# Kernel tuning notes

Measured on AMD Instinct MI355X. Metric: run time of the kernel, lower is better.

The kernel has to match this reference:

```python
import jax, jax.numpy as jnp
import numpy as np

B, N, F, H = 4, 1024, 1024, 16
D = F // H  # head_dim = 64


def setup_inputs() -> dict:
    key = jax.random.key(0)
    ks = jax.random.split(key, 12)
    s = 1.0 / np.sqrt(F)
    return {
        "feature_map": jax.random.normal(ks[0], (B, N, F), jnp.float32),
        "scene_token": jax.random.normal(ks[1], (B, F), jnp.float32),
        "relation_matrix": jax.random.normal(ks[2], (2 * N, 2 * N), jnp.float32) * 0.05,
        "Wq": jax.random.normal(ks[3], (F, F), jnp.float32) * s,
        "bq": jnp.zeros((F,), jnp.float32),
        "Wk": jax.random.normal(ks[4], (F, F), jnp.float32) * s,
        "bk": jnp.zeros((F,), jnp.float32),
        "Wv": jax.random.normal(ks[5], (F, F), jnp.float32) * s,
        "bv": jnp.zeros((F,), jnp.float32),
        "Wo": jax.random.normal(ks[6], (F, F), jnp.float32) * s,
        "bo": jnp.zeros((F,), jnp.float32),
    }


def reference(feature_map, scene_token, relation_matrix, Wq, bq, Wk, bk, Wv, bv, Wo, bo):
    b, n, f = feature_map.shape
    # scene token broadcast to n copies, concatenated -> [b, 2n, f]
    scene = jnp.broadcast_to(scene_token[:, None, :], (b, n, f))
    x = jnp.concatenate([scene, feature_map], axis=1)  # [b, 2n, f]
    q = (x @ Wq.T + bq).reshape(b, -1, H, D)
    k = (x @ Wk.T + bk).reshape(b, -1, H, D)
    v = (x @ Wv.T + bv).reshape(b, -1, H, D)
    scores = jnp.einsum("bqhd,bkhd->bhqk", q, k) / jnp.sqrt(jnp.float32(D))
    scores = scores + relation_matrix[None, None, :, :]
    weights = jax.nn.softmax(scores, axis=-1)
    attn = jnp.einsum("bhqk,bkhd->bqhd", weights, v).reshape(b, -1, f)
    return attn @ Wo.T + bo
```

## Files before the change

kernel.cpp:

```cpp
#include <hip/hip_runtime.h>
#include <hip/hip_bf16.h>
#include <cstdint>

typedef __hip_bfloat16 bf16;
typedef __attribute__((ext_vector_type(8))) short short8;
typedef __attribute__((ext_vector_type(4))) float f32x4;
typedef __attribute__((ext_vector_type(2))) unsigned int uint2v;

#define MFMA16(a, b, c) __builtin_amdgcn_mfma_f32_16x16x32_bf16((a), (b), (c), 0, 0, 0)

__device__ __forceinline__ void gl2lds16(const void* g, void* l) {
  __builtin_amdgcn_global_load_lds(
      (const __attribute__((address_space(1))) unsigned int*)g,
      (__attribute__((address_space(3))) unsigned int*)l,
      16, 0, 0);
}

__device__ __forceinline__ unsigned int pkcvt(float a, float b) {
  unsigned int r;
  asm("v_cvt_pk_bf16_f32 %0, %1, %2" : "=v"(r) : "v"(a), "v"(b));
  return r;
}

__device__ __forceinline__ uint2v plswap32(unsigned a, unsigned b) {
#if __has_builtin(__builtin_amdgcn_permlane32_swap)
  return __builtin_amdgcn_permlane32_swap(a, b, false, false);
#else
  const unsigned ax = __shfl_xor((int)a, 32), bx = __shfl_xor((int)b, 32);
  const bool hi = (threadIdx.x & 32) != 0;
  uint2v r;
  r[0] = hi ? bx : a;
  r[1] = hi ? b : ax;
  return r;
#endif
}

__device__ __forceinline__ uint2v plswap16(unsigned a, unsigned b) {
#if __has_builtin(__builtin_amdgcn_permlane16_swap)
  return __builtin_amdgcn_permlane16_swap(a, b, false, false);
#else
  const unsigned ax = __shfl_xor((int)a, 16), bx = __shfl_xor((int)b, 16);
  const bool hi = (threadIdx.x & 16) != 0;
  uint2v r;
  r[0] = hi ? bx : a;
  r[1] = hi ? b : ax;
  return r;
#endif
}

template <int V> struct IC { static constexpr int value = V; };

template <int WRITE_BF16>
__global__ __launch_bounds__(256) void gemm_bt(
    const bf16* __restrict__ A, const bf16* __restrict__ Bt,
    const float* __restrict__ bias, bf16* __restrict__ outb,
    float* __restrict__ outf, int M, int N, int K) {
  __shared__ bf16 sA[128 * 64];
  __shared__ bf16 sB[128 * 64];
  const int tid = threadIdx.x, w = tid >> 6, lane = tid & 63;
  const int n16 = lane & 15, quad = lane >> 4;
  const int mBase = blockIdx.y * 128, nBase = blockIdx.x * 128;
  const int wr = w >> 1, wc = w & 1;

  f32x4 acc[4][4];
#pragma unroll
  for (int mi = 0; mi < 4; mi++)
#pragma unroll
    for (int ni = 0; ni < 4; ni++) acc[mi][ni] = (f32x4){0.f, 0.f, 0.f, 0.f};

  const bf16* ag[4];
  const bf16* bg[4];
#pragma unroll
  for (int i = 0; i < 4; i++) {
    const int e = (i * 256 + tid) * 8;
    const int row = e >> 6, c0 = e & 63;
    const int col = c0 ^ ((row & 7) << 3);
    ag[i] = A + (size_t)(mBase + row) * K + col;
    bg[i] = Bt + (size_t)(nBase + row) * K + col;
  }
  const int u = (quad * 16) ^ ((n16 & 7) << 4);
  const int a0 = (wr * 64 + n16) * 128 + u;
  const int b0 = (wc * 64 + n16) * 128 + u;
  const char* const sAB = (const char*)sA;
  const char* const sBB = (const char*)sB;

  for (int k0 = 0; k0 < K; k0 += 64) {
    __syncthreads();
#pragma unroll
    for (int i = 0; i < 4; i++) {
      gl2lds16(ag[i] + k0, sA + i * 2048 + w * 512);
      gl2lds16(bg[i] + k0, sB + i * 2048 + w * 512);
    }
    __syncthreads();

#pragma unroll
    for (int kk = 0; kk < 2; kk++) {
      short8 af[4], bfg[4];
#pragma unroll
      for (int t = 0; t < 4; t++) {
        af[t] = *(const short8*)(sAB + (a0 ^ (kk << 6)) + t * 2048);
        bfg[t] = *(const short8*)(sBB + (b0 ^ (kk << 6)) + t * 2048);
      }
#pragma unroll
      for (int mi = 0; mi < 4; mi++)
#pragma unroll
        for (int ni = 0; ni < 4; ni++)
          acc[mi][ni] = MFMA16(af[mi], bfg[ni], acc[mi][ni]);
    }
  }

#pragma unroll
  for (int mi = 0; mi < 4; mi++)
#pragma unroll
    for (int ni = 0; ni < 4; ni++)
#pragma unroll
      for (int r = 0; r < 4; r++) {
        const int row = mBase + wr * 64 + mi * 16 + quad * 4 + r;
        const int col = nBase + wc * 64 + ni * 16 + n16;
        const float v = acc[mi][ni][r] + bias[col];
        if (WRITE_BF16)
          outb[(size_t)row * N + col] = __float2bfloat16(v);
        else
          outf[(size_t)row * N + col] = v;
      }
}

__global__ __launch_bounds__(256) void flash_kernel(
    const bf16* __restrict__ qkv, const float* __restrict__ relf,
    bf16* __restrict__ attn) {
  constexpr int S = 2048, R3 = 3072;
  __shared__ __align__(16) char smem[32768];
  bf16* const sK = (bf16*)smem;
  char* const sVtB = smem + 16384;

  const int tid = threadIdx.x, w = tid >> 6, lane = tid & 63;
  const int n16 = lane & 15, quad = lane >> 4;
  const int qt = blockIdx.x & 15;
  const int bh = blockIdx.x >> 4;
  const int h = bh & 15, b = bh >> 4;
  const int qb = qt * 128 + w * 32;
  const size_t rowbase = (size_t)b * S;
  const float SC = 0.125f * 1.44269504f;
  const size_t TADV = (size_t)64 * R3;

  short8 qf[2][2];
#pragma unroll
  for (int mi = 0; mi < 2; mi++) {
    const bf16* qp = qkv + (rowbase + qb + mi * 16 + n16) * R3 + h * 64;
#pragma unroll
    for (int c = 0; c < 2; c++) qf[mi][c] = *(const short8*)(qp + c * 32 + quad * 8);
  }

  f32x4 ot[4][2];
#pragma unroll
  for (int nc = 0; nc < 4; nc++)
#pragma unroll
    for (int mi = 0; mi < 2; mi++) ot[nc][mi] = (f32x4){0.f, 0.f, 0.f, 0.f};
  float l_lane[2] = {0.f, 0.f};

  const bf16* kg0;
  const bf16* kg1;
  {
    const int e0 = tid * 8;
    const int e1 = (256 + tid) * 8;
    const int k0r = e0 >> 6, c00 = e0 & 63;
    const int k1r = e1 >> 6, c01 = e1 & 63;
    kg0 = qkv + (rowbase + k0r) * R3 + 1024 + h * 64 + (c00 ^ ((k0r & 7) << 3));
    kg1 = qkv + (rowbase + k1r) * R3 + 1024 + h * 64 + (c01 ^ ((k1r & 7) << 3));
  }
  const int kldsoff = w * 512;

  const int kb0 = n16 * 128 + ((quad * 16) ^ ((n16 & 7) << 4));
  const int kb1 = kb0 ^ 64;
  const char* const sKB = (const char*)sK;

  const int kp = lane & 31;
  const int vd0 = w * 16 + (lane >> 5) * 8;
  const int kp4 = kp * 4;
  const bf16* vp = qkv + (rowbase + 2 * kp) * R3 + 2048 + h * 64 + vd0;

  const int vb0 = 128 * n16 + ((16 * quad) ^ ((n16 & 7) << 4));
  const int vb1 = vb0 ^ 64;

  short8 v0, v1;
  auto vstage = [&](int bufbyte) {
    const unsigned* a1 = (const unsigned*)&v1;
    const unsigned* a0 = (const unsigned*)&v0;
#pragma unroll
    for (int j = 0; j < 4; j++) {
      const unsigned lo = __builtin_amdgcn_perm(a1[j], a0[j], 0x05040100u);
      const unsigned hi = __builtin_amdgcn_perm(a1[j], a0[j], 0x07060302u);
      *(unsigned*)(sVtB + bufbyte + 128 * (vd0 + 2 * j) + (kp4 ^ ((2 * j) << 4))) = lo;
      *(unsigned*)(sVtB + bufbyte + 128 * (vd0 + 2 * j + 1) + (kp4 ^ ((2 * j + 1) << 4))) = hi;
    }
  };

  gl2lds16(kg0, sK + kldsoff);
  gl2lds16(kg1, sK + kldsoff + 2048);
  kg0 += TADV;
  kg1 += TADV;

  v0 = *(const short8*)vp;
  v1 = *(const short8*)(vp + R3);
  vstage(0);
  vp += TADV;
  v0 = *(const short8*)vp;
  v1 = *(const short8*)(vp + R3);
  vp += TADV;

  float4 rv[8];
  const float4* rpA = (const float4*)relf + (size_t)(qt * 32) * 2048 + w * 512 + lane;
  const float4* rpB = rpA + 256;
#pragma unroll
  for (int j = 0; j < 4; j++) {
    rv[j] = rpA[j * 64];
    rv[4 + j] = rpB[j * 64];
  }
  rpA += 2048;
  rpB += 2048;

  auto step = [&](auto curc, bool dodma, bool dovpf) {
    constexpr int CUR = decltype(curc)::value;
    constexpr int NXT = CUR ^ 1;
    __syncthreads();

    if (dodma) {
      gl2lds16(kg0, sK + NXT * 4096 + kldsoff);
      kg0 += TADV;
      gl2lds16(kg1, sK + NXT * 4096 + kldsoff + 2048);
      kg1 += TADV;
      vstage(NXT * 8192);
    }

#pragma unroll
    for (int kc = 0; kc < 2; kc++) {
      f32x4 st[2][2];
#pragma unroll
      for (int t2 = 0; t2 < 2; t2++) {
        const int kt4 = 2 * kc + t2;
        short8 kf[2];
        kf[0] = *(const short8*)(sKB + CUR * 8192 + kt4 * 2048 + kb0);
        kf[1] = *(const short8*)(sKB + CUR * 8192 + kt4 * 2048 + kb1);
#pragma unroll
        for (int mi = 0; mi < 2; mi++) {
          f32x4 z = (f32x4){0.f, 0.f, 0.f, 0.f};
          z = MFMA16(kf[0], qf[mi][0], z);
          z = MFMA16(kf[1], qf[mi][1], z);
          st[t2][mi] = z;
        }
      }
      if (kc == 0 && dovpf) {
        v0 = *(const short8*)vp;
        v1 = *(const short8*)(vp + R3);
        vp += TADV;
      }
      short8 pb[2];
#pragma unroll
      for (int mi = 0; mi < 2; mi++) {
        float acc = 0.f;
        unsigned d[2][2];
#pragma unroll
        for (int t2 = 0; t2 < 2; t2++) {
          const float4 rr = rv[mi * 4 + 2 * kc + t2];
          float p0 = __builtin_amdgcn_exp2f(fmaf(st[t2][mi][0], SC, rr.x));
          float p1 = __builtin_amdgcn_exp2f(fmaf(st[t2][mi][1], SC, rr.y));
          float p2 = __builtin_amdgcn_exp2f(fmaf(st[t2][mi][2], SC, rr.z));
          float p3 = __builtin_amdgcn_exp2f(fmaf(st[t2][mi][3], SC, rr.w));
          acc += (p0 + p1) + (p2 + p3);
          d[t2][0] = pkcvt(p0, p1);
          d[t2][1] = pkcvt(p2, p3);
        }
        l_lane[mi] += acc;
        const uint2v e0 = plswap32(d[0][0], d[1][0]);
        const uint2v e1 = plswap32(d[0][1], d[1][1]);
        const uint2v f0 = plswap16(e0[0], e0[1]);
        const uint2v f1 = plswap16(e1[0], e1[1]);
        union { short8 s; unsigned u[4]; } P;
        P.u[0] = f0[0]; P.u[1] = f1[0]; P.u[2] = f0[1]; P.u[3] = f1[1];
        pb[mi] = P.s;
      }
      if (kc == 1 && dodma) {
#pragma unroll
        for (int j = 0; j < 4; j++) {
          rv[j] = rpA[j * 64];
          rv[4 + j] = rpB[j * 64];
        }
        rpA += 2048;
        rpB += 2048;
      }
      short8 va[4];
#pragma unroll
      for (int nc = 0; nc < 4; nc++)
        va[nc] = *(const short8*)(sVtB + CUR * 8192 + 2048 * nc +
                                  (kc ? vb1 : vb0));
#pragma unroll
      for (int nc = 0; nc < 4; nc++)
#pragma unroll
        for (int mi = 0; mi < 2; mi++)
          ot[nc][mi] = MFMA16(va[nc], pb[mi], ot[nc][mi]);
    }
  };

#pragma unroll 1
  for (int t = 0; t < 16; t++) {
    const bool g = (t < 15);
    step(IC<0>{}, true, g);
    step(IC<1>{}, g, g);
  }

  float inv[2];
#pragma unroll
  for (int mi = 0; mi < 2; mi++) {
    float l = l_lane[mi];
    l += __shfl_xor(l, 16);
    l += __shfl_xor(l, 32);
    inv[mi] = 1.0f / l;
  }
  __syncthreads();
  bf16* const sEp = (bf16*)smem + w * (32 * 72);
#pragma unroll
  for (int mi = 0; mi < 2; mi++)
#pragma unroll
    for (int nc = 0; nc < 4; nc++) {
      uint2 pk;
      pk.x = pkcvt(ot[nc][mi][0] * inv[mi], ot[nc][mi][1] * inv[mi]);
      pk.y = pkcvt(ot[nc][mi][2] * inv[mi], ot[nc][mi][3] * inv[mi]);
      *(uint2*)(&sEp[(mi * 16 + n16) * 72 + nc * 16 + quad * 4]) = pk;
    }
#pragma unroll
  for (int t = 0; t < 4; t++) {
    const int row = t * 8 + (lane >> 3);
    const int dcol = (lane & 7) * 8;
    const short8 vrow = *(const short8*)(&sEp[row * 72 + dcol]);
    *(short8*)(attn + (rowbase + qb + row) * 1024 + h * 64 + dcol) = vrow;
  }
}

__global__ void prep_main(const float* __restrict__ fm, const float* __restrict__ scene,
                          const float* __restrict__ Wq, const float* __restrict__ Wk,
                          const float* __restrict__ Wv, const float* __restrict__ Wo,
                          const float* __restrict__ bq, const float* __restrict__ bk,
                          const float* __restrict__ bv, bf16* __restrict__ wW,
                          bf16* __restrict__ wWo, float* __restrict__ bC,
                          bf16* __restrict__ x) {
  const int blk = blockIdx.x;
  if (blk < 4096) {
    const int sel = blk >> 10;
    const int i = (((blk & 1023) * 256) + threadIdx.x) * 4;
    const float* src = (sel == 0) ? Wq : (sel == 1) ? Wk : (sel == 2) ? Wv : Wo;
    bf16* dst = (sel < 3) ? (wW + ((size_t)sel << 20) + i) : (wWo + i);
    const float4 v = *(const float4*)(src + i);
    dst[0] = __float2bfloat16(v.x);
    dst[1] = __float2bfloat16(v.y);
    dst[2] = __float2bfloat16(v.z);
    dst[3] = __float2bfloat16(v.w);
    if (blk == 0) {
      for (int z = threadIdx.x; z < 3072; z += 256)
        bC[z] = (z < 1024) ? bq[z] : (z < 2048) ? bk[z - 1024] : bv[z - 2048];
    }
  } else {
    const int bx = blk - 4096;
    const size_t i = ((size_t)bx * 256 + threadIdx.x) * 4;
    const int r = (int)(i >> 10), c = (int)(i & 1023);
    const int b = r >> 11, s = r & 2047;
    const float* src = (s < 1024)
                           ? (scene + ((size_t)b << 10) + c)
                           : (fm + (((size_t)b * 1024 + (s - 1024)) << 10) + c);
    const float4 v = *(const float4*)src;
    bf16* d = x + i;
    d[0] = __float2bfloat16(v.x);
    d[1] = __float2bfloat16(v.y);
    d[2] = __float2bfloat16(v.z);
    d[3] = __float2bfloat16(v.w);
  }
}

__global__ void prep_rel(const float* __restrict__ rel, float* __restrict__ relf) {
  const int idx = blockIdx.x * 256 + threadIdx.x;
  const int lane = idx & 63;
  const int j = (idx >> 6) & 7;
  const int w = (idx >> 9) & 3;
  const int kt = (idx >> 11) & 31;
  const int qt = idx >> 16;
  const int n16 = lane & 15, quad = lane >> 4;
  const int mi = j >> 2, kt4 = j & 3;
  const int qrow = qt * 128 + w * 32 + mi * 16 + n16;
  const int key = kt * 64 + kt4 * 16 + quad * 4;
  const float L2E = 1.44269504f;
  float4 v = *(const float4*)(rel + (size_t)qrow * 2048 + key);
  v.x *= L2E; v.y *= L2E; v.z *= L2E; v.w *= L2E;
  ((float4*)relf)[idx] = v;
}

extern "C" void kernel_launch(void* const* d_in, const int* in_sizes, int n_in,
                              void* d_out, int out_size, void* d_ws,
                              size_t ws_size, hipStream_t stream) {
  const float* fm    = (const float*)d_in[0];
  const float* scene = (const float*)d_in[1];
  const float* rel   = (const float*)d_in[2];
  const float* Wq    = (const float*)d_in[3];
  const float* bq    = (const float*)d_in[4];
  const float* Wk    = (const float*)d_in[5];
  const float* bk    = (const float*)d_in[6];
  const float* Wv    = (const float*)d_in[7];
  const float* bv    = (const float*)d_in[8];
  const float* Wo    = (const float*)d_in[9];
  const float* bo    = (const float*)d_in[10];
  float* out = (float*)d_out;

  char* ws = (char*)d_ws;
  bf16* x    = (bf16*)(ws);
  float* relf = (float*)(ws);
  bf16* qkv  = (bf16*)(ws + (16u << 20));
  bf16* attn = (bf16*)(ws + (64u << 20));
  bf16* wW   = (bf16*)(ws + (80u << 20));
  bf16* wWo  = (bf16*)(ws + (86u << 20));
  float* bC  = (float*)(ws + (88u << 20));

  prep_main<<<12288, 256, 0, stream>>>(fm, scene, Wq, Wk, Wv, Wo, bq, bk, bv,
                                       wW, wWo, bC, x);

  gemm_bt<1><<<dim3(24, 64), 256, 0, stream>>>(x, wW, bC, qkv, nullptr,
                                               8192, 3072, 1024);
  prep_rel<<<4096, 256, 0, stream>>>(rel, relf);
  flash_kernel<<<1024, 256, 0, stream>>>(qkv, relf, attn);
  gemm_bt<0><<<dim3(8, 64), 256, 0, stream>>>(attn, wWo, bo, nullptr, out,
                                              8192, 1024, 1024);
}
```

Before: 311.1 us.

## Replace GEMM with 256x128-tile, 512-thread, triple-buffered pipelined kernel

Replaces the 128x128 single-buffered GEMM with a 256x128 tile kernel of 8 waves that uses 144KB of dynamic LDS as a triple buffer. Global-to-LDS loads for tile t+2 are issued between the two halves of the MFMA work, with explicit vmcnt waits, s_barrier, and setprio raised around the MFMA blocks. The goal is to hide global memory latency behind compute and remove the two full syncthreads per k-step. The trade is large LDS use, which limits the kernel to one block per CU, and K is now hard-coded to 1024.

```diff
diff --git a/kernel.cpp b/kernel.cpp
--- a/kernel.cpp
+++ b/kernel.cpp
@@ -8,6 +8,7 @@
 typedef __attribute__((ext_vector_type(2))) unsigned int uint2v;
 
 #define MFMA16(a, b, c) __builtin_amdgcn_mfma_f32_16x16x32_bf16((a), (b), (c), 0, 0, 0)
+#define SBAR() asm volatile("s_barrier" ::: "memory")
 
 __device__ __forceinline__ void gl2lds16(const void* g, void* l) {
   __builtin_amdgcn_global_load_lds(
@@ -51,72 +52,120 @@
 template <int V> struct IC { static constexpr int value = V; };
 
 template <int WRITE_BF16>
-__global__ __launch_bounds__(256) void gemm_bt(
+__global__ __launch_bounds__(512) void gemm256(
     const bf16* __restrict__ A, const bf16* __restrict__ Bt,
     const float* __restrict__ bias, bf16* __restrict__ outb,
-    float* __restrict__ outf, int M, int N, int K) {
-  __shared__ bf16 sA[128 * 64];
-  __shared__ bf16 sB[128 * 64];
+    float* __restrict__ outf, int M, int N) {
+  constexpr int K = 1024, NT = 16;
+  extern __shared__ char smem[];
+  bf16* const sAe = (bf16*)smem;
+  bf16* const sBe = (bf16*)(smem + 98304);
+  const char* const sAB = (const char*)smem;
+  const char* const sBB = (const char*)(smem + 98304);
+
   const int tid = threadIdx.x, w = tid >> 6, lane = tid & 63;
   const int n16 = lane & 15, quad = lane >> 4;
-  const int mBase = blockIdx.y * 128, nBase = blockIdx.x * 128;
-  const int wr = w >> 1, wc = w & 1;
-
-  f32x4 acc[4][4];
-#pragma unroll
-  for (int mi = 0; mi < 4; mi++)
-#pragma unroll
-    for (int ni = 0; ni < 4; ni++) acc[mi][ni] = (f32x4){0.f, 0.f, 0.f, 0.f};
-
-  const bf16* ag[4];
-  const bf16* bg[4];
-#pragma unroll
-  for (int i = 0; i < 4; i++) {
-    const int e = (i * 256 + tid) * 8;
-    const int row = e >> 6, c0 = e & 63;
-    const int col = c0 ^ ((row & 7) << 3);
-    ag[i] = A + (size_t)(mBase + row) * K + col;
-    bg[i] = Bt + (size_t)(nBase + row) * K + col;
-  }
-  const int u = (quad * 16) ^ ((n16 & 7) << 4);
-  const int a0 = (wr * 64 + n16) * 128 + u;
-  const int b0 = (wc * 64 + n16) * 128 + u;
-  const char* const sAB = (const char*)sA;
-  const char* const sBB = (const char*)sB;
-
-  for (int k0 = 0; k0 < K; k0 += 64) {
-    __syncthreads();
-#pragma unroll
-    for (int i = 0; i < 4; i++) {
-      gl2lds16(ag[i] + k0, sA + i * 2048 + w * 512);
-      gl2lds16(bg[i] + k0, sB + i * 2048 + w * 512);
-    }
-    __syncthreads();
-
-#pragma unroll
-    for (int kk = 0; kk < 2; kk++) {
-      short8 af[4], bfg[4];
-#pragma unroll
-      for (int t = 0; t < 4; t++) {
-        af[t] = *(const short8*)(sAB + (a0 ^ (kk << 6)) + t * 2048);
-        bfg[t] = *(const short8*)(sBB + (b0 ^ (kk << 6)) + t * 2048);
-      }
+  const int wm = w >> 2, wn = w & 3;
+  const int bm = blockIdx.y * 256, bn = blockIdx.x * 128;
+
+  f32x4 acc[8][2];
+#pragma unroll
+  for (int mi = 0; mi < 8; mi++)
+#pragma unroll
+    for (int ni = 0; ni < 2; ni++) acc[mi][ni] = (f32x4){0.f, 0.f, 0.f, 0.f};
+
+  const int srow = tid >> 3;
+  const int scol = ((tid & 7) * 8) ^ ((srow & 7) << 3);
+  const bf16* const pA = A + (size_t)(bm + srow) * K + scol;
+  const bf16* const pB = Bt + (size_t)(bn + srow) * K + scol;
+
+  const int sw = (quad * 16) ^ ((n16 & 7) << 4);
+  const int abase = (wm * 128 + n16) * 128 + sw;
+  const int bbase = (wn * 32 + n16) * 128 + sw;
+
+  auto stA = [&](int buf, int s, int t) {
+    gl2lds16(pA + (size_t)(s * 64) * K + t * 64,
+             sAe + buf * 16384 + s * 4096 + w * 512);
+  };
+  auto stB = [&](int buf, int s, int t) {
+    gl2lds16(pB + (size_t)(s * 64) * K + t * 64,
+             sBe + buf * 8192 + s * 4096 + w * 512);
+  };
+
+#pragma unroll
+  for (int s = 0; s < 4; s++) stA(0, s, 0);
+#pragma unroll
+  for (int s = 0; s < 2; s++) stB(0, s, 0);
+#pragma unroll
+  for (int s = 0; s < 4; s++) stA(1, s, 1);
+#pragma unroll
+  for (int s = 0; s < 2; s++) stB(1, s, 1);
+  asm volatile("s_waitcnt vmcnt(6)" ::: "memory");
+  SBAR();
+
+#pragma unroll
+  for (int t = 0; t < NT; ++t) {
+    const int buf = t % 3, nb = (t + 2) % 3;
+    const bool st = (t < NT - 2);
+
+    short8 bfr[2][2], af[4][2];
+#pragma unroll
+    for (int ni = 0; ni < 2; ni++)
+#pragma unroll
+      for (int kk = 0; kk < 2; kk++)
+        bfr[ni][kk] = *(const short8*)(sBB + buf * 16384 + ni * 2048 +
+                                       (bbase ^ (kk << 6)));
+#pragma unroll
+    for (int mi = 0; mi < 4; mi++)
+#pragma unroll
+      for (int kk = 0; kk < 2; kk++)
+        af[mi][kk] = *(const short8*)(sAB + buf * 32768 + mi * 2048 +
+                                      (abase ^ (kk << 6)));
+    if (st) { stA(nb, 0, t + 2); stA(nb, 1, t + 2); stB(nb, 0, t + 2); }
+    SBAR();
+    __builtin_amdgcn_s_setprio(1);
+#pragma unroll
+    for (int kk = 0; kk < 2; kk++)
 #pragma unroll
       for (int mi = 0; mi < 4; mi++)
 #pragma unroll
-        for (int ni = 0; ni < 4; ni++)
-          acc[mi][ni] = MFMA16(af[mi], bfg[ni], acc[mi][ni]);
-    }
-  }
-
-#pragma unroll
-  for (int mi = 0; mi < 4; mi++)
-#pragma unroll
-    for (int ni = 0; ni < 4; ni++)
+        for (int ni = 0; ni < 2; ni++)
+          acc[mi][ni] = MFMA16(af[mi][kk], bfr[ni][kk], acc[mi][ni]);
+    __builtin_amdgcn_s_setprio(0);
+    SBAR();
+
+#pragma unroll
+    for (int mi = 0; mi < 4; mi++)
+#pragma unroll
+      for (int kk = 0; kk < 2; kk++)
+        af[mi][kk] = *(const short8*)(sAB + buf * 32768 + (mi + 4) * 2048 +
+                                      (abase ^ (kk << 6)));
+    if (st) { stA(nb, 2, t + 2); stA(nb, 3, t + 2); stB(nb, 1, t + 2); }
+    SBAR();
+    __builtin_amdgcn_s_setprio(1);
+#pragma unroll
+    for (int kk = 0; kk < 2; kk++)
+#pragma unroll
+      for (int mi = 0; mi < 4; mi++)
+#pragma unroll
+        for (int ni = 0; ni < 2; ni++)
+          acc[mi + 4][ni] = MFMA16(af[mi][kk], bfr[ni][kk], acc[mi + 4][ni]);
+    __builtin_amdgcn_s_setprio(0);
+    if (t < NT - 2)
+      asm volatile("s_waitcnt vmcnt(6)" ::: "memory");
+    else if (t == NT - 2)
+      asm volatile("s_waitcnt vmcnt(0)" ::: "memory");
+    SBAR();
+  }
+
+#pragma unroll
+  for (int mi = 0; mi < 8; mi++)
+#pragma unroll
+    for (int ni = 0; ni < 2; ni++)
 #pragma unroll
       for (int r = 0; r < 4; r++) {
-        const int row = mBase + wr * 64 + mi * 16 + quad * 4 + r;
-        const int col = nBase + wc * 64 + ni * 16 + n16;
+        const int row = bm + wm * 128 + mi * 16 + quad * 4 + r;
+        const int col = bn + wn * 32 + ni * 16 + n16;
         const float v = acc[mi][ni][r] + bias[col];
         if (WRITE_BF16)
           outb[(size_t)row * N + col] = __float2bfloat16(v);
@@ -420,10 +469,10 @@
   prep_main<<<12288, 256, 0, stream>>>(fm, scene, Wq, Wk, Wv, Wo, bq, bk, bv,
                                        wW, wWo, bC, x);
 
-  gemm_bt<1><<<dim3(24, 64), 256, 0, stream>>>(x, wW, bC, qkv, nullptr,
-                                               8192, 3072, 1024);
+  gemm256<1><<<dim3(24, 32), 512, 147456, stream>>>(x, wW, bC, qkv, nullptr,
+                                                    8192, 3072);
   prep_rel<<<4096, 256, 0, stream>>>(rel, relf);
   flash_kernel<<<1024, 256, 0, stream>>>(qkv, relf, attn);
-  gemm_bt<0><<<dim3(8, 64), 256, 0, stream>>>(attn, wWo, bo, nullptr, out,
-                                              8192, 1024, 1024);
-}
+  gemm256<0><<<dim3(8, 32), 512, 147456, stream>>>(attn, wWo, bo, nullptr, out,
+                                                   8192, 1024);
+}
```

Result: slower. 326.7 us (+5.0%).

## Triple-buffer GEMM LDS tiles with async global-to-LDS prefetch pipeline

Applied to the files above, without the earlier changes.

The bf16 GEMM main loop changes from a single 64-wide K tile, synchronised twice per iteration, to a three-stage ring of 32-wide K tiles. Loads are issued two tiles ahead and waited on with explicit vmcnt and s_barrier. The aim is to overlap global-to-LDS transfers with MFMA work and remove the per-iteration full syncthreads stall. The cost is a new swizzled layout, hand-written waitcnt logic that must match the number of issued loads, and smaller K tiles with more barriers overall.

```diff
diff --git a/kernel.cpp b/kernel.cpp
--- a/kernel.cpp
+++ b/kernel.cpp
@@ -8,6 +8,8 @@
 typedef __attribute__((ext_vector_type(2))) unsigned int uint2v;
 
 #define MFMA16(a, b, c) __builtin_amdgcn_mfma_f32_16x16x32_bf16((a), (b), (c), 0, 0, 0)
+#define SBAR() asm volatile("s_barrier" ::: "memory")
+#define VMCNT(n) asm volatile("s_waitcnt vmcnt(" #n ")" ::: "memory")
 
 __device__ __forceinline__ void gl2lds16(const void* g, void* l) {
   __builtin_amdgcn_global_load_lds(
@@ -55,8 +57,10 @@
     const bf16* __restrict__ A, const bf16* __restrict__ Bt,
     const float* __restrict__ bias, bf16* __restrict__ outb,
     float* __restrict__ outf, int M, int N, int K) {
-  __shared__ bf16 sA[128 * 64];
-  __shared__ bf16 sB[128 * 64];
+  __shared__ bf16 sA[3 * 128 * 32];
+  __shared__ bf16 sB[3 * 128 * 32];
+  const char* const sAB = (const char*)sA;
+  const char* const sBB = (const char*)sB;
   const int tid = threadIdx.x, w = tid >> 6, lane = tid & 63;
   const int n16 = lane & 15, quad = lane >> 4;
   const int mBase = blockIdx.y * 128, nBase = blockIdx.x * 128;
@@ -68,45 +72,65 @@
 #pragma unroll
     for (int ni = 0; ni < 4; ni++) acc[mi][ni] = (f32x4){0.f, 0.f, 0.f, 0.f};
 
-  const bf16* ag[4];
-  const bf16* bg[4];
-#pragma unroll
-  for (int i = 0; i < 4; i++) {
-    const int e = (i * 256 + tid) * 8;
-    const int row = e >> 6, c0 = e & 63;
-    const int col = c0 ^ ((row & 7) << 3);
-    ag[i] = A + (size_t)(mBase + row) * K + col;
-    bg[i] = Bt + (size_t)(nBase + row) * K + col;
-  }
-  const int u = (quad * 16) ^ ((n16 & 7) << 4);
-  const int a0 = (wr * 64 + n16) * 128 + u;
-  const int b0 = (wc * 64 + n16) * 128 + u;
-  const char* const sAB = (const char*)sA;
-  const char* const sBB = (const char*)sB;
-
-  for (int k0 = 0; k0 < K; k0 += 64) {
-    __syncthreads();
-#pragma unroll
-    for (int i = 0; i < 4; i++) {
-      gl2lds16(ag[i] + k0, sA + i * 2048 + w * 512);
-      gl2lds16(bg[i] + k0, sB + i * 2048 + w * 512);
-    }
-    __syncthreads();
-
-#pragma unroll
-    for (int kk = 0; kk < 2; kk++) {
-      short8 af[4], bfg[4];
-#pragma unroll
-      for (int t = 0; t < 4; t++) {
-        af[t] = *(const short8*)(sAB + (a0 ^ (kk << 6)) + t * 2048);
-        bfg[t] = *(const short8*)(sBB + (b0 ^ (kk << 6)) + t * 2048);
-      }
-#pragma unroll
-      for (int mi = 0; mi < 4; mi++)
-#pragma unroll
-        for (int ni = 0; ni < 4; ni++)
-          acc[mi][ni] = MFMA16(af[mi], bfg[ni], acc[mi][ni]);
-    }
+  const bf16* ag[2];
+  const bf16* bg[2];
+#pragma unroll
+  for (int i = 0; i < 2; i++) {
+    const int E = (i * 256 + tid) * 8;
+    const int j = E >> 6;
+    const int v = (E & 63) * 2;
+    const int u = v ^ ((j & 7) << 4);
+    const int row = 2 * j + (u >> 6);
+    const int kcol = (u & 63) >> 1;
+    ag[i] = A + (size_t)(mBase + row) * K + kcol;
+    bg[i] = Bt + (size_t)(nBase + row) * K + kcol;
+  }
+  const int jj = n16 >> 1;
+  const int u0 = ((n16 & 1) * 64 + quad * 16) ^ (jj << 4);
+  const int aRd = (wr * 32 + jj) * 128 + u0;
+  const int bRd = (wc * 32 + jj) * 128 + u0;
+
+  auto stage = [&](int buf, int kt) {
+#pragma unroll
+    for (int i = 0; i < 2; i++) {
+      gl2lds16(ag[i] + kt * 32, sA + buf * 4096 + i * 2048 + w * 512);
+      gl2lds16(bg[i] + kt * 32, sB + buf * 4096 + i * 2048 + w * 512);
+    }
+  };
+
+  const int NT = K >> 5;
+  stage(0, 0);
+  stage(1, 1);
+  VMCNT(4);
+  SBAR();
+
+  int cur = 0;
+  for (int t = 0; t < NT; ++t) {
+    const int nb = (cur == 0) ? 2 : cur - 1;
+    if (t + 2 < NT) stage(nb, t + 2);
+
+    const char* pa = sAB + cur * 8192 + aRd;
+    const char* pb = sBB + cur * 8192 + bRd;
+    short8 af[4], bfg[4];
+#pragma unroll
+    for (int t4 = 0; t4 < 4; t4++) {
+      af[t4] = *(const short8*)(pa + t4 * 1024);
+      bfg[t4] = *(const short8*)(pb + t4 * 1024);
+    }
+#pragma unroll
+    for (int mi = 0; mi < 4; mi++)
+#pragma unroll
+      for (int ni = 0; ni < 4; ni++)
+        acc[mi][ni] = MFMA16(af[mi], bfg[ni], acc[mi][ni]);
+
+    if (t + 2 < NT) {
+      VMCNT(4);
+      SBAR();
+    } else if (t + 1 < NT) {
+      VMCNT(0);
+      SBAR();
+    }
+    cur = (cur == 2) ? 0 : cur + 1;
   }
 
 #pragma unroll
```

Result: slower. 324.8 us (+4.4%).

## Exploit broadcast scene rows: collapse duplicate keys and compute scene QKV once

Applied to the files above, without the earlier changes.

The first 1024 sequence positions are copies of the scene token, so their Q/K/V rows are identical. The scene QKV is now computed once per batch with a small GEMV and broadcast into the qkv buffer, which halves the main QKV GEMM. Feature-row queries attend to the 1024 identical scene keys through a single key whose weight is the exp of the q·k score times a precomputed per-row sum of exp(relation). That halves their key loop in the flash kernel. The price is three extra small kernels and a non-max-subtracted exp term for the collapsed key, which can lose precision if scores are large.

```diff
diff --git a/kernel.cpp b/kernel.cpp
--- a/kernel.cpp
+++ b/kernel.cpp
@@ -20,6 +20,12 @@
   unsigned int r;
   asm("v_cvt_pk_bf16_f32 %0, %1, %2" : "=v"(r) : "v"(a), "v"(b));
   return r;
+}
+
+__device__ __forceinline__ float b2f(unsigned short u) {
+  union { unsigned u; float f; } x;
+  x.u = ((unsigned)u) << 16;
+  return x.f;
 }
 
 __device__ __forceinline__ uint2v plswap32(unsigned a, unsigned b) {
@@ -50,7 +56,7 @@
 
 template <int V> struct IC { static constexpr int value = V; };
 
-template <int WRITE_BF16>
+template <int WRITE_BF16, int REMAP>
 __global__ __launch_bounds__(256) void gemm_bt(
     const bf16* __restrict__ A, const bf16* __restrict__ Bt,
     const float* __restrict__ bias, bf16* __restrict__ outb,
@@ -117,17 +123,20 @@
       for (int r = 0; r < 4; r++) {
         const int row = mBase + wr * 64 + mi * 16 + quad * 4 + r;
         const int col = nBase + wc * 64 + ni * 16 + n16;
+        const size_t orow =
+            REMAP ? (size_t)((row >> 10) * 2048 + 1024 + (row & 1023))
+                  : (size_t)row;
         const float v = acc[mi][ni][r] + bias[col];
         if (WRITE_BF16)
-          outb[(size_t)row * N + col] = __float2bfloat16(v);
+          outb[orow * N + col] = __float2bfloat16(v);
         else
-          outf[(size_t)row * N + col] = v;
+          outf[orow * N + col] = v;
       }
 }
 
 __global__ __launch_bounds__(256) void flash_kernel(
     const bf16* __restrict__ qkv, const float* __restrict__ relf,
-    bf16* __restrict__ attn) {
+    bf16* __restrict__ attn, const float* __restrict__ lR1) {
   constexpr int S = 2048, R3 = 3072;
   __shared__ __align__(16) char smem[32768];
   bf16* const sK = (bf16*)smem;
@@ -140,6 +149,8 @@
   const int h = bh & 15, b = bh >> 4;
   const int qb = qt * 128 + w * 32;
   const size_t rowbase = (size_t)b * S;
+  const bool isFeat = (qt >= 8);
+  const size_t krow0 = rowbase + (isFeat ? 1024 : 0);
   const float SC = 0.125f * 1.44269504f;
   const size_t TADV = (size_t)64 * R3;
 
@@ -162,11 +173,11 @@
   const bf16* kg1;
   {
     const int e0 = tid * 8;
-    const int e1 = (256 + tid) * 8;
+    const int e1i = (256 + tid) * 8;
     const int k0r = e0 >> 6, c00 = e0 & 63;
-    const int k1r = e1 >> 6, c01 = e1 & 63;
-    kg0 = qkv + (rowbase + k0r) * R3 + 1024 + h * 64 + (c00 ^ ((k0r & 7) << 3));
-    kg1 = qkv + (rowbase + k1r) * R3 + 1024 + h * 64 + (c01 ^ ((k1r & 7) << 3));
+    const int k1r = e1i >> 6, c01 = e1i & 63;
+    kg0 = qkv + (krow0 + k0r) * R3 + 1024 + h * 64 + (c00 ^ ((k0r & 7) << 3));
+    kg1 = qkv + (krow0 + k1r) * R3 + 1024 + h * 64 + (c01 ^ ((k1r & 7) << 3));
   }
   const int kldsoff = w * 512;
 
@@ -177,7 +188,7 @@
   const int kp = lane & 31;
   const int vd0 = w * 16 + (lane >> 5) * 8;
   const int kp4 = kp * 4;
-  const bf16* vp = qkv + (rowbase + 2 * kp) * R3 + 2048 + h * 64 + vd0;
+  const bf16* vp = qkv + (krow0 + 2 * kp) * R3 + 2048 + h * 64 + vd0;
 
   const int vb0 = 128 * n16 + ((16 * quad) ^ ((n16 & 7) << 4));
   const int vb1 = vb0 ^ 64;
@@ -209,7 +220,8 @@
   vp += TADV;
 
   float4 rv[8];
-  const float4* rpA = (const float4*)relf + (size_t)(qt * 32) * 2048 + w * 512 + lane;
+  const float4* rpA = (const float4*)relf +
+                      (size_t)(qt * 32 + (isFeat ? 16 : 0)) * 2048 + w * 512 + lane;
   const float4* rpB = rpA + 256;
 #pragma unroll
   for (int j = 0; j < 4; j++) {
@@ -301,11 +313,50 @@
     }
   };
 
+  const int NP = isFeat ? 8 : 16;
 #pragma unroll 1
-  for (int t = 0; t < 16; t++) {
-    const bool g = (t < 15);
+  for (int t = 0; t < NP; t++) {
+    const bool g = (t < NP - 1);
     step(IC<0>{}, true, g);
     step(IC<1>{}, g, g);
+  }
+
+  if (isFeat) {
+    const bf16* kscp = qkv + rowbase * R3 + 1024 + h * 64 + quad * 8;
+    const short8 ks0 = *(const short8*)(kscp);
+    const short8 ks1 = *(const short8*)(kscp + 32);
+    float e1v[2];
+#pragma unroll
+    for (int mi = 0; mi < 2; mi++) {
+      float ss = 0.f;
+#pragma unroll
+      for (int j = 0; j < 8; j++) {
+        ss = fmaf(b2f((unsigned short)qf[mi][0][j]), b2f((unsigned short)ks0[j]), ss);
+        ss = fmaf(b2f((unsigned short)qf[mi][1][j]), b2f((unsigned short)ks1[j]), ss);
+      }
+      ss += __shfl_xor(ss, 16);
+      ss += __shfl_xor(ss, 32);
+      const float lr = lR1[qb - 1024 + mi * 16 + n16];
+      e1v[mi] = __builtin_amdgcn_exp2f(fmaf(ss, SC, lr));
+      if (quad == 0) l_lane[mi] += e1v[mi];
+    }
+    const bf16* vscp = qkv + rowbase * R3 + 2048 + h * 64;
+#pragma unroll
+    for (int nc = 0; nc < 4; nc++) {
+      const int d0 = nc * 16 + quad * 4;
+      const uint2 vv = *(const uint2*)(vscp + d0);
+      const float w0 = b2f((unsigned short)(vv.x & 0xffff));
+      const float w1 = b2f((unsigned short)(vv.x >> 16));
+      const float w2 = b2f((unsigned short)(vv.y & 0xffff));
+      const float w3 = b2f((unsigned short)(vv.y >> 16));
+#pragma unroll
+      for (int mi = 0; mi < 2; mi++) {
+        ot[nc][mi][0] = fmaf(e1v[mi], w0, ot[nc][mi][0]);
+        ot[nc][mi][1] = fmaf(e1v[mi], w1, ot[nc][mi][1]);
+        ot[nc][mi][2] = fmaf(e1v[mi], w2, ot[nc][mi][2]);
+        ot[nc][mi][3] = fmaf(e1v[mi], w3, ot[nc][mi][3]);
+      }
+    }
   }
 
   float inv[2];
@@ -336,13 +387,12 @@
   }
 }
 
-__global__ void prep_main(const float* __restrict__ fm, const float* __restrict__ scene,
-                          const float* __restrict__ Wq, const float* __restrict__ Wk,
-                          const float* __restrict__ Wv, const float* __restrict__ Wo,
-                          const float* __restrict__ bq, const float* __restrict__ bk,
-                          const float* __restrict__ bv, bf16* __restrict__ wW,
-                          bf16* __restrict__ wWo, float* __restrict__ bC,
-                          bf16* __restrict__ x) {
+__global__ void prep_main(const float* __restrict__ fm, const float* __restrict__ Wq,
+                          const float* __restrict__ Wk, const float* __restrict__ Wv,
+                          const float* __restrict__ Wo, const float* __restrict__ bq,
+                          const float* __restrict__ bk, const float* __restrict__ bv,
+                          bf16* __restrict__ wW, bf16* __restrict__ wWo,
+                          float* __restrict__ bC, bf16* __restrict__ x) {
   const int blk = blockIdx.x;
   if (blk < 4096) {
     const int sel = blk >> 10;
@@ -359,20 +409,71 @@
         bC[z] = (z < 1024) ? bq[z] : (z < 2048) ? bk[z - 1024] : bv[z - 2048];
     }
   } else {
-    const int bx = blk - 4096;
-    const size_t i = ((size_t)bx * 256 + threadIdx.x) * 4;
-    const int r = (int)(i >> 10), c = (int)(i & 1023);
-    const int b = r >> 11, s = r & 2047;
-    const float* src = (s < 1024)
-                           ? (scene + ((size_t)b << 10) + c)
-                           : (fm + (((size_t)b * 1024 + (s - 1024)) << 10) + c);
-    const float4 v = *(const float4*)src;
+    const size_t i = ((size_t)(blk - 4096) * 256 + threadIdx.x) * 4;
+    const float4 v = *(const float4*)(fm + i);
     bf16* d = x + i;
     d[0] = __float2bfloat16(v.x);
     d[1] = __float2bfloat16(v.y);
     d[2] = __float2bfloat16(v.z);
     d[3] = __float2bfloat16(v.w);
   }
+}
+
+__global__ void scene_qkv(const float* __restrict__ scene,
+                          const bf16* __restrict__ wW,
+                          const float* __restrict__ bC, bf16* __restrict__ sqv) {
+  const int tid = threadIdx.x;
+  const int p = blockIdx.x * 16 + (tid >> 4);
+  const int i16 = tid & 15;
+  const int b = p / 3072, j = p % 3072;
+  const bf16* wr = wW + (size_t)j * 1024 + i16 * 64;
+  const float* sr = scene + (size_t)b * 1024 + i16 * 64;
+  float s = 0.f;
+#pragma unroll
+  for (int t = 0; t < 8; t++) {
+    const short8 wv = *(const short8*)(wr + t * 8);
+    const float4 x0 = *(const float4*)(sr + t * 8);
+    const float4 x1 = *(const float4*)(sr + t * 8 + 4);
+    const float xs[8] = {x0.x, x0.y, x0.z, x0.w, x1.x, x1.y, x1.z, x1.w};
+#pragma unroll
+    for (int e = 0; e < 8; e++) {
+      const float xb = __bfloat162float(__float2bfloat16(xs[e]));
+      s = fmaf(b2f((unsigned short)wv[e]), xb, s);
+    }
+  }
+  s += __shfl_xor(s, 1);
+  s += __shfl_xor(s, 2);
+  s += __shfl_xor(s, 4);
+  s += __shfl_xor(s, 8);
+  if (i16 == 0) sqv[(size_t)b * 3072 + j] = __float2bfloat16(s + bC[j]);
+}
+
+__global__ void bcast_scene(const bf16* __restrict__ sqv, bf16* __restrict__ qkv) {
+  const int gid = blockIdx.x * 256 + threadIdx.x;
+  const int ri = gid / 384, c8 = gid % 384;
+  const int b = ri >> 10, s = ri & 1023;
+  const uint4 v = *(const uint4*)(sqv + (size_t)b * 3072 + c8 * 8);
+  *(uint4*)(qkv + ((size_t)b * 2048 + s) * 3072 + c8 * 8) = v;
+}
+
+__global__ void prep_r1(const float* __restrict__ rel, float* __restrict__ lR1) {
+  __shared__ float red[4];
+  const int q = 1024 + blockIdx.x;
+  const int tid = threadIdx.x;
+  const float4 v = *(const float4*)(rel + (size_t)q * 2048 + tid * 4);
+  const float L2E = 1.44269504f;
+  float s = __builtin_amdgcn_exp2f(v.x * L2E) + __builtin_amdgcn_exp2f(v.y * L2E) +
+            __builtin_amdgcn_exp2f(v.z * L2E) + __builtin_amdgcn_exp2f(v.w * L2E);
+  s += __shfl_xor(s, 1);
+  s += __shfl_xor(s, 2);
+  s += __shfl_xor(s, 4);
+  s += __shfl_xor(s, 8);
+  s += __shfl_xor(s, 16);
+  s += __shfl_xor(s, 32);
+  if ((tid & 63) == 0) red[tid >> 6] = s;
+  __syncthreads();
+  if (tid == 0)
+    lR1[blockIdx.x] = __builtin_amdgcn_logf((red[0] + red[1]) + (red[2] + red[3]));
 }
 
 __global__ void prep_rel(const float* __restrict__ rel, float* __restrict__ relf) {
@@ -416,14 +517,18 @@
   bf16* wW   = (bf16*)(ws + (80u << 20));
   bf16* wWo  = (bf16*)(ws + (86u << 20));
   float* bC  = (float*)(ws + (88u << 20));
-
-  prep_main<<<12288, 256, 0, stream>>>(fm, scene, Wq, Wk, Wv, Wo, bq, bk, bv,
-                                       wW, wWo, bC, x);
-
-  gemm_bt<1><<<dim3(24, 64), 256, 0, stream>>>(x, wW, bC, qkv, nullptr,
-                                               8192, 3072, 1024);
+  float* lR1 = (float*)(ws + (88u << 20) + 16384);
+  bf16* sqv  = (bf16*)(ws + (88u << 20) + 24576);
+
+  prep_main<<<8192, 256, 0, stream>>>(fm, Wq, Wk, Wv, Wo, bq, bk, bv,
+                                      wW, wWo, bC, x);
+  scene_qkv<<<768, 256, 0, stream>>>(scene, wW, bC, sqv);
+  gemm_bt<1, 1><<<dim3(24, 32), 256, 0, stream>>>(x, wW, bC, qkv, nullptr,
+                                                  4096, 3072, 1024);
+  bcast_scene<<<6144, 256, 0, stream>>>(sqv, qkv);
   prep_rel<<<4096, 256, 0, stream>>>(rel, relf);
-  flash_kernel<<<1024, 256, 0, stream>>>(qkv, relf, attn);
-  gemm_bt<0><<<dim3(8, 64), 256, 0, stream>>>(attn, wWo, bo, nullptr, out,
-                                              8192, 1024, 1024);
-}
+  prep_r1<<<1024, 256, 0, stream>>>(rel, lR1);
+  flash_kernel<<<1024, 256, 0, stream>>>(qkv, relf, attn, lR1);
+  gemm_bt<0, 0><<<dim3(8, 64), 256, 0, stream>>>(attn, wWo, bo, nullptr, out,
+                                                 8192, 1024, 1024);
+}
```

Measured after the change: 319.4 us. 1.03x slower.
